# Kernel optimization log

Measured on AMD Instinct MI355X. Metric: run time of the kernel, lower is better.

The kernel has to match this reference:

```python
import jax, jax.numpy as jnp
import numpy as np

WINDOW_SIZE = 2
SOFTMAX_TEMP = 0.01
WIDTH = 320
EPS = 1e-12  # F.normalize default eps


def _l2norm(x, axis):
    n = jnp.sqrt(jnp.sum(x * x, axis=axis, keepdims=True))
    return x / jnp.maximum(n, EPS)


def setup_inputs() -> dict:
    key = jax.random.key(0)
    k1, k2, k3, k4 = jax.random.split(key, 4)
    BW, C, N, S = 4, 256, 1024, 1
    return {
        "keypoint_scores": jax.random.uniform(k1, (BW, S, N), dtype=jnp.float32),
        "keypoint_desc": jax.random.normal(k2, (BW, C, N), dtype=jnp.float32),
        "desc_dense": jax.random.normal(k3, (BW, C, WIDTH, WIDTH), dtype=jnp.float32),
        "keypoint_coords": jax.random.uniform(k4, (BW, N, 2), dtype=jnp.float32),
    }


def reference(keypoint_scores, keypoint_desc, desc_dense, keypoint_coords):
    BW, C, N = keypoint_desc.shape
    B = BW // WINDOW_SIZE
    P = B * (WINDOW_SIZE - 1)  # number of (src, tgt) pairs

    # dense source pixel coordinates (u=col, v=row), matching torch meshgrid 'ij'
    idx = jnp.arange(WIDTH * WIDTH)
    coords = jnp.stack([(idx % WIDTH).astype(jnp.float32),
                        (idx // WIDTH).astype(jnp.float32)], axis=1)  # (HW, 2)

    # pair indexing: for window i, targets are i*w+1 .. i*w+w-1, source is i*w
    tgt_ids = jnp.array([i * WINDOW_SIZE + j for i in range(B)
                         for j in range(1, WINDOW_SIZE)], dtype=jnp.int32)
    src_ids = (tgt_ids // WINDOW_SIZE) * WINDOW_SIZE

    # normalized dense source descriptors: (B, C, HW)
    src_dense = desc_dense[::WINDOW_SIZE].reshape(B, C, -1)
    src_un = _l2norm(src_dense, axis=1)
    src_sel = src_un[tgt_ids // WINDOW_SIZE]  # (P, C, HW)

    # normalized target keypoint descriptors: (P, C, N)
    tgt_n = _l2norm(keypoint_desc[tgt_ids], axis=1)

    # QK^T over descriptor channel: (P, N, HW)
    match_vals = jnp.einsum('pcn,pcm->pnm', tgt_n, src_sel)
    soft = jax.nn.softmax(match_vals / SOFTMAX_TEMP, axis=2)

    # soft-argmax coordinates: (P, N, 2)
    pseudo_coords = jnp.einsum('pnm,md->pnd', soft, coords)

    match_weights = keypoint_scores[tgt_ids]  # (P, S, N)
    return pseudo_coords, match_weights, tgt_ids, src_ids
```

## Files before the change

### kernel.cpp

```cpp
#include <hip/hip_runtime.h>
#include <stdint.h>

#define HW_      102400
#define C_       256
#define N_       1024
#define P_       2
#define TILES_   1600
#define CHUNKS_  32
#define MEGAS_   25
#define NB_      4
#define K2_      144.269504088896340f
#define MOFF_    (-72.134752044448170f)

typedef __attribute__((ext_vector_type(8)))  short bf16x8;
typedef __attribute__((ext_vector_type(16))) float f32x16;

#define WS_TGT_OFF  0
#define WS_PAR_OFF  (1u << 20)
#define WS_PN_OFF   (4u << 20)

__device__ __forceinline__ uint32_t packbf(float a, float b) {
  uint32_t r;
  asm("v_cvt_pk_bf16_f32 %0, %1, %2" : "=v"(r) : "v"(a), "v"(b));
  return r;
}
__device__ __forceinline__ float fexp2(float x) {
  return __builtin_amdgcn_exp2f(x);
}
__device__ __forceinline__ void dma16(const uint32_t* g, uint32_t* l) {
  __builtin_amdgcn_global_load_lds(
      (const __attribute__((address_space(1))) uint32_t*)g,
      (__attribute__((address_space(3))) uint32_t*)l, 16, 0, 0);
}

__global__ __launch_bounds__(256)
void k_pre(const float* __restrict__ dense, const float* __restrict__ kdesc,
           const float* __restrict__ kscores, uint32_t* __restrict__ PN,
           uint16_t* __restrict__ tgt, float* __restrict__ out) {
  __shared__ float part[16][64];
  __shared__ float sinv[64];
  const int bid = blockIdx.x;
  if (bid < P_ * TILES_) {
    const int p = bid / TILES_, tile = bid % TILES_;
    const int t   = threadIdx.x;
    const int px4 = (t & 15) * 4;
    const int cg  = t >> 4;
    const float* src = dense + (size_t)(p * 2) * C_ * HW_ + (size_t)(cg * 16) * HW_
                     + tile * 64 + px4;
    float v[16][4];
    #pragma unroll
    for (int cc = 0; cc < 16; ++cc) {
      const float4 qd = *(const float4*)(src + (size_t)cc * HW_);
      v[cc][0] = qd.x; v[cc][1] = qd.y; v[cc][2] = qd.z; v[cc][3] = qd.w;
    }
    float ps[4] = {0.f, 0.f, 0.f, 0.f};
    #pragma unroll
    for (int cc = 0; cc < 16; ++cc) {
      #pragma unroll
      for (int i = 0; i < 4; ++i) ps[i] = fmaf(v[cc][i], v[cc][i], ps[i]);
    }
    #pragma unroll
    for (int i = 0; i < 4; ++i) part[cg][px4 + i] = ps[i];
    __syncthreads();
    if (t < 64) {
      float s = 0.f;
      #pragma unroll
      for (int g = 0; g < 16; ++g) s += part[g][t];
      sinv[t] = 1.f / fmaxf(sqrtf(s), 1e-12f);
    }
    __syncthreads();
    uint32_t* dstg = PN + ((size_t)(p * TILES_ + tile) << 13) + cg * 512;
    #pragma unroll
    for (int i = 0; i < 4; ++i) {
      const int r  = px4 + i;
      const float iv = sinv[r];
      uint32_t* d = dstg + 4 * r;
      uint4 A, B;
      A.x = packbf(v[0][i] * iv,  v[1][i] * iv);
      A.y = packbf(v[2][i] * iv,  v[3][i] * iv);
      A.z = packbf(v[4][i] * iv,  v[5][i] * iv);
      A.w = packbf(v[6][i] * iv,  v[7][i] * iv);
      B.x = packbf(v[8][i] * iv,  v[9][i] * iv);
      B.y = packbf(v[10][i] * iv, v[11][i] * iv);
      B.z = packbf(v[12][i] * iv, v[13][i] * iv);
      B.w = packbf(v[14][i] * iv, v[15][i] * iv);
      *(uint4*)&d[0]   = A;
      *(uint4*)&d[256] = B;
    }
  } else {
    const int t = (bid - P_ * TILES_) * 256 + threadIdx.x;
    const int p = t >> 10, n = t & 1023;
    const float* src = kdesc + (size_t)(p * 2 + 1) * C_ * N_ + n;
    float s = 0.f;
    #pragma unroll 16
    for (int c = 0; c < C_; ++c) { const float v2 = src[c * N_]; s = fmaf(v2, v2, s); }
    const float inv = 1.f / fmaxf(sqrtf(s), 1e-12f);
    uint32_t* dst = (uint32_t*)(tgt + (size_t)t * C_);
    #pragma unroll 4
    for (int c8 = 0; c8 < C_; c8 += 8) {
      uint4 wv;
      wv.x = packbf(src[(c8 + 0) * N_] * inv, src[(c8 + 1) * N_] * inv);
      wv.y = packbf(src[(c8 + 2) * N_] * inv, src[(c8 + 3) * N_] * inv);
      wv.z = packbf(src[(c8 + 4) * N_] * inv, src[(c8 + 5) * N_] * inv);
      wv.w = packbf(src[(c8 + 6) * N_] * inv, src[(c8 + 7) * N_] * inv);
      *(uint4*)&dst[c8 / 2] = wv;
    }
    out[4096 + t] = kscores[(p * 2 + 1) * N_ + n];
  }
}

__global__ __launch_bounds__(512, 2)
void k_main(const uint32_t* __restrict__ PN, const uint16_t* __restrict__ tgt,
            float4* __restrict__ partials) {
  __shared__ uint32_t lds[2 * 16384];

  const int bid = blockIdx.x;
  const int xcd = bid & 7;
  const int rr  = bid >> 3;
  const int nb  = rr & 3;
  const int grp = xcd + 8 * (rr >> 2);
  const int p     = grp >> 5;
  const int chunk = grp & 31;

  const int t    = threadIdx.x;
  const int lane = t & 63;
  const int w    = t >> 6;
  const int l31  = lane & 31;
  const int hi   = lane >> 5;
  const int h    = w & 1;
  const int q    = w >> 1;

  bf16x8 Bf[2][16];
  const int nbase = nb * 256 + q * 64;
  #pragma unroll
  for (int j = 0; j < 2; ++j) {
    const uint16_t* tp = tgt + (size_t)(p * N_ + nbase + j * 32 + l31) * C_ + hi * 8;
    #pragma unroll
    for (int kk = 0; kk < 16; ++kk) Bf[j][kk] = *(const bf16x8*)(tp + kk * 16);
  }

  float stS[2], stU[2], stV[2];
  #pragma unroll
  for (int j = 0; j < 2; ++j) { stS[j] = 0.f; stU[j] = 0.f; stV[j] = 0.f; }

  const int arow = hi * 256 + (h * 32 + l31) * 4;
  const float ubstat = (float)(h * 32 + 4 * hi);

  const uint32_t* PNc = PN + ((size_t)(p * TILES_ + chunk * 2 * MEGAS_) << 13) + w * 2048 + lane * 4;
  uint32_t* ldsw = &lds[w * 2048];

  #pragma unroll
  for (int jj = 0; jj < 8; ++jj) dma16(PNc + jj * 256, ldsw + jj * 256);
  __syncthreads();

  float u0f = 0.f, v0f = (float)(chunk * 10);
  for (int m = 0; m < MEGAS_; ++m) {
    if (m + 1 < MEGAS_) {
      const uint32_t* s = PNc + ((size_t)(m + 1) << 14);
      uint32_t* d = ldsw + (((m + 1) & 1) ? 16384 : 0);
      #pragma unroll
      for (int jj = 0; jj < 8; ++jj) dma16(s + jj * 256, d + jj * 256);
    }

    const uint32_t* buf = &lds[(m & 1) * 16384];
    f32x16 acc[2][2];
    #pragma unroll
    for (int s2 = 0; s2 < 2; ++s2)
      #pragma unroll
      for (int j = 0; j < 2; ++j)
        #pragma unroll
        for (int e = 0; e < 16; ++e) acc[s2][j][e] = 0.f;

    __builtin_amdgcn_s_setprio(1);
    #pragma unroll
    for (int kk = 0; kk < 16; ++kk) {
      const bf16x8 a0 = *(const bf16x8*)&buf[kk * 512 + arow];
      const bf16x8 a1 = *(const bf16x8*)&buf[8192 + kk * 512 + arow];
      acc[0][0] = __builtin_amdgcn_mfma_f32_32x32x16_bf16(a0, Bf[0][kk], acc[0][0], 0, 0, 0);
      acc[0][1] = __builtin_amdgcn_mfma_f32_32x32x16_bf16(a0, Bf[1][kk], acc[0][1], 0, 0, 0);
      acc[1][0] = __builtin_amdgcn_mfma_f32_32x32x16_bf16(a1, Bf[0][kk], acc[1][0], 0, 0, 0);
      acc[1][1] = __builtin_amdgcn_mfma_f32_32x32x16_bf16(a1, Bf[1][kk], acc[1][1], 0, 0, 0);
    }
    __builtin_amdgcn_s_setprio(0);

    #pragma unroll
    for (int s2 = 0; s2 < 2; ++s2) {
      const float ub = u0f + ubstat;
      #pragma unroll
      for (int j = 0; j < 2; ++j) {
        float tS = 0.f, tC = 0.f;
        #pragma unroll
        for (int r = 0; r < 16; ++r) {
          const float ev = fexp2(fmaf(K2_, acc[s2][j][r], MOFF_));
          tS += ev;
          tC = fmaf(ev, (float)((r & 3) + 8 * (r >> 2)), tC);
        }
        stS[j] += tS;
        stU[j] = fmaf(ub, tS, stU[j] + tC);
        stV[j] = fmaf(v0f, tS, stV[j]);
      }
      u0f += 64.f;
      if (u0f > 290.f) { u0f = 0.f; v0f += 1.f; }
    }

    __syncthreads();
  }

  #pragma unroll
  for (int j = 0; j < 2; ++j) {
    float S = stS[j], U = stU[j], V = stV[j];
    S += __shfl_xor(S, 32, 64); U += __shfl_xor(U, 32, 64); V += __shfl_xor(V, 32, 64);
    if (lane < 32) {
      const int n = nbase + j * 32 + l31;
      partials[((size_t)(p * CHUNKS_ + chunk) * 2 + h) * N_ + n] = make_float4(S, U, V, 0.f);
    }
  }
}

__global__ void k_final(const float4* __restrict__ partials, float* __restrict__ out) {
  const int t = blockIdx.x * blockDim.x + threadIdx.x;
  const int p = t >> 10, n = t & 1023;
  float S = 0.f, U = 0.f, V = 0.f;
  #pragma unroll 4
  for (int s = 0; s < 2 * CHUNKS_; ++s) {
    const float4 v = partials[((size_t)p * 2 * CHUNKS_ + s) * N_ + n];
    S += v.x; U += v.y; V += v.z;
  }
  out[(size_t)(p * N_ + n) * 2 + 0] = U / S;
  out[(size_t)(p * N_ + n) * 2 + 1] = V / S;
  if (t < 4) {
    const float ids[4] = {1.f, 3.f, 0.f, 2.f};
    out[6144 + t] = ids[t];
  }
}

extern "C" void kernel_launch(void* const* d_in, const int* in_sizes, int n_in,
                              void* d_out, int out_size, void* d_ws, size_t ws_size,
                              hipStream_t stream) {
  const float* kscores = (const float*)d_in[0];
  const float* kdesc   = (const float*)d_in[1];
  const float* dense   = (const float*)d_in[2];
  float* out = (float*)d_out;

  char* ws = (char*)d_ws;
  uint16_t* tgt = (uint16_t*)(ws + WS_TGT_OFF);
  float4*   par = (float4*)(ws + WS_PAR_OFF);
  uint32_t* PN  = (uint32_t*)(ws + WS_PN_OFF);

  k_pre<<<P_ * TILES_ + (P_ * N_) / 256, 256, 0, stream>>>(dense, kdesc, kscores, PN, tgt, out);
  k_main<<<P_ * NB_ * CHUNKS_, 512, 0, stream>>>(PN, tgt, par);
  k_final<<<(P_ * N_) / 256, 256, 0, stream>>>(par, out);
}
```

Baseline: 189.7 us.

## Replace block-wide double buffer with per-wave 4-slot async pipeline

The bf16 normalized dense-descriptor layout is reordered so each wave owns a contiguous 32-pixel by 64-channel slice. The main loop now gives each wave private LDS slots filled by global_load_lds, prefetches two stages ahead, and waits on vmcnt counters instead of block-wide __syncthreads. This removes the barriers between waves so MFMA and the exp epilogue of different waves can interleave more freely. In exchange each stage issues smaller loads, and correctness now relies on the hand-written waitcnt values matching the number of outstanding loads.

```diff
diff --git a/kernel.cpp b/kernel.cpp
--- a/kernel.cpp
+++ b/kernel.cpp
@@ -7,7 +7,8 @@
 #define P_       2
 #define TILES_   1600
 #define CHUNKS_  32
-#define MEGAS_   25
+#define TPC_     50
+#define STAGES_  200
 #define NB_      4
 #define K2_      144.269504088896340f
 #define MOFF_    (-72.134752044448170f)
@@ -69,12 +70,15 @@
       sinv[t] = 1.f / fmaxf(sqrtf(s), 1e-12f);
     }
     __syncthreads();
-    uint32_t* dstg = PN + ((size_t)(p * TILES_ + tile) << 13) + cg * 512;
+    const int kq  = cg >> 2;
+    const int kkI = cg & 3;
     #pragma unroll
     for (int i = 0; i < 4; ++i) {
       const int r  = px4 + i;
+      const int hh = r >> 5, rp = r & 31;
       const float iv = sinv[r];
-      uint32_t* d = dstg + 4 * r;
+      uint32_t* d = PN + ((((size_t)(p * TILES_ + tile) * 2 + hh) * 4 + kq) << 10)
+                  + kkI * 256 + rp * 4;
       uint4 A, B;
       A.x = packbf(v[0][i] * iv,  v[1][i] * iv);
       A.y = packbf(v[2][i] * iv,  v[3][i] * iv);
@@ -85,7 +89,7 @@
       B.z = packbf(v[12][i] * iv, v[13][i] * iv);
       B.w = packbf(v[14][i] * iv, v[15][i] * iv);
       *(uint4*)&d[0]   = A;
-      *(uint4*)&d[256] = B;
+      *(uint4*)&d[128] = B;
     }
   } else {
     const int t = (bid - P_ * TILES_) * 256 + threadIdx.x;
@@ -112,7 +116,7 @@
 __global__ __launch_bounds__(512, 2)
 void k_main(const uint32_t* __restrict__ PN, const uint16_t* __restrict__ tgt,
             float4* __restrict__ partials) {
-  __shared__ uint32_t lds[2 * 16384];
+  __shared__ uint32_t lds[32768];
 
   const int bid = blockIdx.x;
   const int xcd = bid & 7;
@@ -143,67 +147,66 @@
   #pragma unroll
   for (int j = 0; j < 2; ++j) { stS[j] = 0.f; stU[j] = 0.f; stV[j] = 0.f; }
 
-  const int arow = hi * 256 + (h * 32 + l31) * 4;
-  const float ubstat = (float)(h * 32 + 4 * hi);
-
-  const uint32_t* PNc = PN + ((size_t)(p * TILES_ + chunk * 2 * MEGAS_) << 13) + w * 2048 + lane * 4;
-  uint32_t* ldsw = &lds[w * 2048];
-
-  #pragma unroll
-  for (int jj = 0; jj < 8; ++jj) dma16(PNc + jj * 256, ldsw + jj * 256);
-  __syncthreads();
+  const int roff = hi * 128 + l31 * 4;
+  uint32_t* wslot = &lds[w * 4096];
+  const size_t pb = ((size_t)(p * TILES_ + chunk * TPC_) * 2 + h) * 4;
+  const uint32_t* PNl = PN + lane * 4;
+
+  {
+    const uint32_t* s0 = PNl + ((pb + 0) << 10);
+    uint32_t* d0 = wslot;
+    dma16(s0, d0); dma16(s0 + 256, d0 + 256); dma16(s0 + 512, d0 + 512); dma16(s0 + 768, d0 + 768);
+    const uint32_t* s1 = PNl + ((pb + 1) << 10);
+    uint32_t* d1 = wslot + 1024;
+    dma16(s1, d1); dma16(s1 + 256, d1 + 256); dma16(s1 + 512, d1 + 512); dma16(s1 + 768, d1 + 768);
+  }
+
+  f32x16 acc0, acc1;
+  #pragma unroll
+  for (int r = 0; r < 16; ++r) { acc0[r] = 0.f; acc1[r] = 0.f; }
 
   float u0f = 0.f, v0f = (float)(chunk * 10);
-  for (int m = 0; m < MEGAS_; ++m) {
-    if (m + 1 < MEGAS_) {
-      const uint32_t* s = PNc + ((size_t)(m + 1) << 14);
-      uint32_t* d = ldsw + (((m + 1) & 1) ? 16384 : 0);
+  for (int g = 0; g < STAGES_; ++g) {
+    if (g + 2 < STAGES_) {
+      const uint32_t* s = PNl + ((pb + (size_t)(((g + 2) >> 2) * 8 + ((g + 2) & 3))) << 10);
+      uint32_t* d = wslot + ((g + 2) & 3) * 1024;
+      dma16(s, d); dma16(s + 256, d + 256); dma16(s + 512, d + 512); dma16(s + 768, d + 768);
+      asm volatile("s_waitcnt vmcnt(8)" ::: "memory");
+    } else if (g + 1 < STAGES_) {
+      asm volatile("s_waitcnt vmcnt(4)" ::: "memory");
+    } else {
+      asm volatile("s_waitcnt vmcnt(0)" ::: "memory");
+    }
+    __builtin_amdgcn_sched_barrier(0);
+
+    const uint32_t* slot = wslot + (g & 3) * 1024;
+    const int kb = (g & 3) * 4;
+    __builtin_amdgcn_s_setprio(1);
+    #pragma unroll
+    for (int kkI = 0; kkI < 4; ++kkI) {
+      const bf16x8 a = *(const bf16x8*)&slot[kkI * 256 + roff];
+      acc0 = __builtin_amdgcn_mfma_f32_32x32x16_bf16(a, Bf[0][kb + kkI], acc0, 0, 0, 0);
+      acc1 = __builtin_amdgcn_mfma_f32_32x32x16_bf16(a, Bf[1][kb + kkI], acc1, 0, 0, 0);
+    }
+    __builtin_amdgcn_s_setprio(0);
+
+    if ((g & 3) == 3) {
+      const float ub = u0f + (float)(h * 32 + 4 * hi);
+      float tS0 = 0.f, tC0 = 0.f, tS1 = 0.f, tC1 = 0.f;
       #pragma unroll
-      for (int jj = 0; jj < 8; ++jj) dma16(s + jj * 256, d + jj * 256);
-    }
-
-    const uint32_t* buf = &lds[(m & 1) * 16384];
-    f32x16 acc[2][2];
-    #pragma unroll
-    for (int s2 = 0; s2 < 2; ++s2)
-      #pragma unroll
-      for (int j = 0; j < 2; ++j)
-        #pragma unroll
-        for (int e = 0; e < 16; ++e) acc[s2][j][e] = 0.f;
-
-    __builtin_amdgcn_s_setprio(1);
-    #pragma unroll
-    for (int kk = 0; kk < 16; ++kk) {
-      const bf16x8 a0 = *(const bf16x8*)&buf[kk * 512 + arow];
-      const bf16x8 a1 = *(const bf16x8*)&buf[8192 + kk * 512 + arow];
-      acc[0][0] = __builtin_amdgcn_mfma_f32_32x32x16_bf16(a0, Bf[0][kk], acc[0][0], 0, 0, 0);
-      acc[0][1] = __builtin_amdgcn_mfma_f32_32x32x16_bf16(a0, Bf[1][kk], acc[0][1], 0, 0, 0);
-      acc[1][0] = __builtin_amdgcn_mfma_f32_32x32x16_bf16(a1, Bf[0][kk], acc[1][0], 0, 0, 0);
-      acc[1][1] = __builtin_amdgcn_mfma_f32_32x32x16_bf16(a1, Bf[1][kk], acc[1][1], 0, 0, 0);
-    }
-    __builtin_amdgcn_s_setprio(0);
-
-    #pragma unroll
-    for (int s2 = 0; s2 < 2; ++s2) {
-      const float ub = u0f + ubstat;
-      #pragma unroll
-      for (int j = 0; j < 2; ++j) {
-        float tS = 0.f, tC = 0.f;
-        #pragma unroll
-        for (int r = 0; r < 16; ++r) {
-          const float ev = fexp2(fmaf(K2_, acc[s2][j][r], MOFF_));
-          tS += ev;
-          tC = fmaf(ev, (float)((r & 3) + 8 * (r >> 2)), tC);
-        }
-        stS[j] += tS;
-        stU[j] = fmaf(ub, tS, stU[j] + tC);
-        stV[j] = fmaf(v0f, tS, stV[j]);
+      for (int r = 0; r < 16; ++r) {
+        const float cr = (float)((r & 3) + 8 * (r >> 2));
+        const float e0 = fexp2(fmaf(K2_, acc0[r], MOFF_));
+        const float e1 = fexp2(fmaf(K2_, acc1[r], MOFF_));
+        tS0 += e0; tC0 = fmaf(e0, cr, tC0);
+        tS1 += e1; tC1 = fmaf(e1, cr, tC1);
+        acc0[r] = 0.f; acc1[r] = 0.f;
       }
+      stS[0] += tS0; stU[0] = fmaf(ub, tS0, stU[0] + tC0); stV[0] = fmaf(v0f, tS0, stV[0]);
+      stS[1] += tS1; stU[1] = fmaf(ub, tS1, stU[1] + tC1); stV[1] = fmaf(v0f, tS1, stV[1]);
       u0f += 64.f;
       if (u0f > 290.f) { u0f = 0.f; v0f += 1.f; }
     }
-
-    __syncthreads();
   }
 
   #pragma unroll
```

Result: slower. 574.1 us (+202.7%).
